# Performance work log

Hardware: AMD Instinct MI355X
Metric: run time of the kernel (lower is better)

Reference implementation:

```python
import jax, jax.numpy as jnp
import numpy as np

N_QUERY, N_POINTS, FEAT_DIM, K = 32768, 8192, 32, 8

def setup_inputs() -> dict:
    key = jax.random.key(0)
    k1, k2, k3 = jax.random.split(key, 3)
    xyz = jax.random.normal(k1, (N_QUERY, 3), dtype=jnp.float32)
    points = jax.random.normal(k2, (N_POINTS, 3), dtype=jnp.float32)
    # neural_point features are initialized uniform(-1e-4, 1e-4) in the module;
    # we use small-scale gaussians of the same magnitude.
    feats = jax.random.normal(k3, (N_POINTS, FEAT_DIM), dtype=jnp.float32) * 1e-4
    return {"xyz": xyz, "points": points, "feats": feats, "k": K}

def reference(xyz, points, feats, k):
    # Brute-force exact KNN (kpknn equivalent): squared euclidean distances [N, P]
    d2 = (jnp.sum(xyz * xyz, axis=-1, keepdims=True)
          - 2.0 * (xyz @ points.T)
          + jnp.sum(points * points, axis=-1)[None, :])
    _, idx = jax.lax.top_k(-d2, k)          # idx: [N, k] nearest-point indices
    knn_points = points[idx]                # [N, k, 3]
    knn_feats = feats[idx]                  # [N, k, FEAT_DIM]
    return knn_points, knn_feats
```

## Files before the change

### kernel.cpp

```cpp
#include <hip/hip_runtime.h>

#define NQ 32768
#define NP 8192
#define FD 32
#define KNN 8
#define QW 4
#define WPB 4
#define TB 256
#define QBLK (QW * WPB)
#define CHP 1024
#define NCH (NP / CHP)
#define ACH 4
#define CAP 64

__global__ __launch_bounds__(TB) void knn_kernel(
    const float* __restrict__ xyz, const float* __restrict__ points,
    const float* __restrict__ feats, float* __restrict__ out)
{
#pragma clang fp contract(off)
    __shared__ float4 sp[CHP];
    __shared__ unsigned short sidx16[QBLK * CAP];
    __shared__ int scnt[QBLK];

    const int t     = threadIdx.x;
    const int lane  = t & 63;
    const int wid   = t >> 6;
    const int qbase = blockIdx.x * QBLK + wid * QW;

    if (t < QBLK) scnt[t] = 0;

    float qx[QW], qy[QW], qz[QW], qn[QW];
#pragma unroll
    for (int qq = 0; qq < QW; ++qq) {
        int q = qbase + qq;
        float a = xyz[q * 3 + 0], b = xyz[q * 3 + 1], c = xyz[q * 3 + 2];
        qx[qq] = a; qy[qq] = b; qz[qq] = c;
        qn[qq] = (a * a + b * b) + c * c;
    }

    float mn[QW];
#pragma unroll
    for (int qq = 0; qq < QW; ++qq) mn[qq] = __builtin_inff();

    for (int c = 0; c < ACH; ++c) {
        __syncthreads();
        for (int i = t; i < CHP; i += TB) {
            int pi = c * CHP + i;
            float px = points[pi * 3 + 0], py = points[pi * 3 + 1], pz = points[pi * 3 + 2];
            float pn = __builtin_fmaf(pz, pz, __builtin_fmaf(py, py, px * px));
            sp[i] = make_float4(px, py, pz, pn);
        }
        __syncthreads();
#pragma unroll 4
        for (int s = 0; s < CHP / 64; ++s) {
            float4 p = sp[s * 64 + lane];
#pragma unroll
            for (int qq = 0; qq < QW; ++qq) {
                float dot = __builtin_fmaf(qz[qq], p.z, __builtin_fmaf(qy[qq], p.y, qx[qq] * p.x));
                float g   = __builtin_fmaf(-2.0f, dot, p.w);
                mn[qq] = fminf(mn[qq], g);
            }
        }
    }

    float tscr[QW];
#pragma unroll
    for (int qq = 0; qq < QW; ++qq) {
        float v = mn[qq];
        for (int k2 = 2; k2 <= 64; k2 <<= 1)
            for (int j = k2 >> 1; j > 0; j >>= 1) {
                float o = __shfl_xor(v, j);
                bool keepMin = ((lane & k2) == 0) == ((lane & j) == 0);
                v = ((o < v) == keepMin) ? o : v;
            }
        float t8 = __uint_as_float((unsigned)__builtin_amdgcn_readlane((int)__float_as_uint(v), 7));
        tscr[qq] = t8 + 1e-3f;
    }

    for (int k = 0; k < NCH; ++k) {
        int c = (ACH - 1 + k) & (NCH - 1);
        if (k > 0) {
            __syncthreads();
            for (int i = t; i < CHP; i += TB) {
                int pi = c * CHP + i;
                float px = points[pi * 3 + 0], py = points[pi * 3 + 1], pz = points[pi * 3 + 2];
                float pn = __builtin_fmaf(pz, pz, __builtin_fmaf(py, py, px * px));
                sp[i] = make_float4(px, py, pz, pn);
            }
            __syncthreads();
        }
#pragma unroll 2
        for (int s = 0; s < CHP / 64; ++s) {
            float4 p = sp[s * 64 + lane];
            int gidx = c * CHP + s * 64 + lane;
#pragma unroll
            for (int qq = 0; qq < QW; ++qq) {
                float dot = __builtin_fmaf(qz[qq], p.z, __builtin_fmaf(qy[qq], p.y, qx[qq] * p.x));
                float g   = __builtin_fmaf(-2.0f, dot, p.w);
                if (__builtin_expect(g <= tscr[qq], 0)) {
                    int wq = wid * QW + qq;
                    int slot = atomicAdd(&scnt[wq], 1);
                    if (slot < CAP) sidx16[wq * CAP + slot] = (unsigned short)gidx;
                }
            }
        }
    }
    __syncthreads();

    const float4* feats4 = (const float4*)feats;
    float4* outf4 = (float4*)(out + (long)NQ * KNN * 3);
#pragma unroll
    for (int qq = 0; qq < QW; ++qq) {
        int wq = wid * QW + qq;
        int cnt = scnt[wq]; if (cnt > CAP) cnt = CAP;
        unsigned long long key = ~0ull;
        if (lane < cnt) {
            int idx = sidx16[wq * CAP + lane];
            float px = points[idx * 3 + 0], py = points[idx * 3 + 1], pz = points[idx * 3 + 2];
            float pn  = (px * px + py * py) + pz * pz;
            float dot = __builtin_fmaf(qz[qq], pz, __builtin_fmaf(qy[qq], py, qx[qq] * px));
            float d2  = (qn[qq] - 2.0f * dot) + pn;
            unsigned b = __float_as_uint(d2);
            unsigned mk = (b & 0x80000000u) ? ~b : (b | 0x80000000u);
            key = ((unsigned long long)mk << 32) | (unsigned)idx;
        }
        for (int k2 = 2; k2 <= 64; k2 <<= 1)
            for (int j = k2 >> 1; j > 0; j >>= 1) {
                unsigned lo = __shfl_xor((unsigned)key, j);
                unsigned hi = __shfl_xor((unsigned)(key >> 32), j);
                unsigned long long o = ((unsigned long long)hi << 32) | lo;
                bool keepMin = ((lane & k2) == 0) == ((lane & j) == 0);
                key = ((o < key) == keepMin) ? o : key;
            }
        int q = qbase + qq;
        int nb = __shfl((int)(unsigned)key, lane >> 3);
        outf4[(long)q * (KNN * FD / 4) + lane] = feats4[(long)nb * (FD / 4) + (lane & 7)];
        int j2 = lane / 3;
        int nb2 = __shfl((int)(unsigned)key, j2);
        if (lane < 24) {
            out[(long)q * (KNN * 3) + lane] = points[nb2 * 3 + (lane - j2 * 3)];
        }
    }
}

extern "C" void kernel_launch(void* const* d_in, const int* in_sizes, int n_in,
                              void* d_out, int out_size, void* d_ws, size_t ws_size,
                              hipStream_t stream) {
    const float* xyz    = (const float*)d_in[0];
    const float* points = (const float*)d_in[1];
    const float* feats  = (const float*)d_in[2];
    float* out = (float*)d_out;
    hipLaunchKernelGGL(knn_kernel, dim3(NQ / QBLK), dim3(TB), 0, stream,
                       xyz, points, feats, out);
}
```

Before: 78.76 us.

## Merge KNN threshold and screening passes, double queries per wave

The kernel drops the separate min-distance pass over four chunks. It now computes a provisional threshold from the first chunk, then screens chunks 1-3 while still refining the running minimum, re-screens chunk 0, and finishes the rest, for nine chunk passes instead of twelve. Queries per wave go from 4 to 8 to reuse each shared-memory point load across more queries. Points are pre-scaled by -2 so each distance is three FMAs. Because the early screening uses a looser threshold, the candidate capacity is raised to 128, with a second bitonic sort and a merge when more than 64 candidates appear. This costs more registers, halves the grid size, and adds extra sort work when there are many candidates.

```diff
diff --git a/kernel.cpp b/kernel.cpp
--- a/kernel.cpp
+++ b/kernel.cpp
@@ -4,14 +4,38 @@
 #define NP 8192
 #define FD 32
 #define KNN 8
-#define QW 4
+#define QW 8
 #define WPB 4
 #define TB 256
 #define QBLK (QW * WPB)
 #define CHP 1024
-#define NCH (NP / CHP)
-#define ACH 4
-#define CAP 64
+#define CAP 128
+
+typedef unsigned long long u64;
+
+__device__ __forceinline__ u64 shfl_xor_u64(u64 k, int j) {
+    unsigned lo = __shfl_xor((unsigned)k, j);
+    unsigned hi = __shfl_xor((unsigned)(k >> 32), j);
+    return ((u64)hi << 32) | lo;
+}
+__device__ __forceinline__ u64 sort64_u64(u64 key, int lane) {
+    for (int k2 = 2; k2 <= 64; k2 <<= 1)
+        for (int j = k2 >> 1; j > 0; j >>= 1) {
+            u64 o = shfl_xor_u64(key, j);
+            bool keepMin = ((lane & k2) == 0) == ((lane & j) == 0);
+            key = ((o < key) == keepMin) ? o : key;
+        }
+    return key;
+}
+__device__ __forceinline__ float eighth_smallest64(float v, int lane) {
+    for (int k2 = 2; k2 <= 64; k2 <<= 1)
+        for (int j = k2 >> 1; j > 0; j >>= 1) {
+            float o = __shfl_xor(v, j);
+            bool keepMin = ((lane & k2) == 0) == ((lane & j) == 0);
+            v = ((o < v) == keepMin) ? o : v;
+        }
+    return __uint_as_float((unsigned)__builtin_amdgcn_readlane((int)__float_as_uint(v), 7));
+}
 
 __global__ __launch_bounds__(TB) void knn_kernel(
     const float* __restrict__ xyz, const float* __restrict__ points,
@@ -29,91 +53,64 @@
 
     if (t < QBLK) scnt[t] = 0;
 
-    float qx[QW], qy[QW], qz[QW], qn[QW];
+    float qx[QW], qy[QW], qz[QW], qn[QW], mn[QW], tscr[QW];
 #pragma unroll
     for (int qq = 0; qq < QW; ++qq) {
         int q = qbase + qq;
         float a = xyz[q * 3 + 0], b = xyz[q * 3 + 1], c = xyz[q * 3 + 2];
         qx[qq] = a; qy[qq] = b; qz[qq] = c;
         qn[qq] = (a * a + b * b) + c * c;
+        mn[qq] = __builtin_inff();
+        tscr[qq] = __builtin_inff();
     }
 
-    float mn[QW];
-#pragma unroll
-    for (int qq = 0; qq < QW; ++qq) mn[qq] = __builtin_inff();
-
-    for (int c = 0; c < ACH; ++c) {
+    for (int step = 0; step < 9; ++step) {
+        int c = (step <= 3) ? step : ((step == 4) ? 0 : step - 1);
         __syncthreads();
         for (int i = t; i < CHP; i += TB) {
             int pi = c * CHP + i;
             float px = points[pi * 3 + 0], py = points[pi * 3 + 1], pz = points[pi * 3 + 2];
             float pn = __builtin_fmaf(pz, pz, __builtin_fmaf(py, py, px * px));
-            sp[i] = make_float4(px, py, pz, pn);
+            sp[i] = make_float4(-2.0f * px, -2.0f * py, -2.0f * pz, pn);
         }
         __syncthreads();
-#pragma unroll 4
-        for (int s = 0; s < CHP / 64; ++s) {
-            float4 p = sp[s * 64 + lane];
-#pragma unroll
-            for (int qq = 0; qq < QW; ++qq) {
-                float dot = __builtin_fmaf(qz[qq], p.z, __builtin_fmaf(qy[qq], p.y, qx[qq] * p.x));
-                float g   = __builtin_fmaf(-2.0f, dot, p.w);
-                mn[qq] = fminf(mn[qq], g);
-            }
-        }
-    }
 
-    float tscr[QW];
-#pragma unroll
-    for (int qq = 0; qq < QW; ++qq) {
-        float v = mn[qq];
-        for (int k2 = 2; k2 <= 64; k2 <<= 1)
-            for (int j = k2 >> 1; j > 0; j >>= 1) {
-                float o = __shfl_xor(v, j);
-                bool keepMin = ((lane & k2) == 0) == ((lane & j) == 0);
-                v = ((o < v) == keepMin) ? o : v;
-            }
-        float t8 = __uint_as_float((unsigned)__builtin_amdgcn_readlane((int)__float_as_uint(v), 7));
-        tscr[qq] = t8 + 1e-3f;
-    }
-
-    for (int k = 0; k < NCH; ++k) {
-        int c = (ACH - 1 + k) & (NCH - 1);
-        if (k > 0) {
-            __syncthreads();
-            for (int i = t; i < CHP; i += TB) {
-                int pi = c * CHP + i;
-                float px = points[pi * 3 + 0], py = points[pi * 3 + 1], pz = points[pi * 3 + 2];
-                float pn = __builtin_fmaf(pz, pz, __builtin_fmaf(py, py, px * px));
-                sp[i] = make_float4(px, py, pz, pn);
-            }
-            __syncthreads();
-        }
+        const bool doMin = (step < 4), doScr = (step != 0);
 #pragma unroll 2
         for (int s = 0; s < CHP / 64; ++s) {
             float4 p = sp[s * 64 + lane];
             int gidx = c * CHP + s * 64 + lane;
 #pragma unroll
             for (int qq = 0; qq < QW; ++qq) {
-                float dot = __builtin_fmaf(qz[qq], p.z, __builtin_fmaf(qy[qq], p.y, qx[qq] * p.x));
-                float g   = __builtin_fmaf(-2.0f, dot, p.w);
-                if (__builtin_expect(g <= tscr[qq], 0)) {
-                    int wq = wid * QW + qq;
-                    int slot = atomicAdd(&scnt[wq], 1);
-                    if (slot < CAP) sidx16[wq * CAP + slot] = (unsigned short)gidx;
+                float g = __builtin_fmaf(qx[qq], p.x,
+                          __builtin_fmaf(qy[qq], p.y,
+                          __builtin_fmaf(qz[qq], p.z, p.w)));
+                if (doMin) mn[qq] = fminf(mn[qq], g);
+                if (doScr) {
+                    if (__builtin_expect(g <= tscr[qq], 0)) {
+                        int wq = wid * QW + qq;
+                        int slot = atomicAdd(&scnt[wq], 1);
+                        if (slot < CAP) sidx16[wq * CAP + slot] = (unsigned short)gidx;
+                    }
                 }
             }
         }
+
+        if (step == 0 || step == 3) {
+#pragma unroll
+            for (int qq = 0; qq < QW; ++qq)
+                tscr[qq] = eighth_smallest64(mn[qq], lane) + 1e-3f;
+        }
     }
-    __syncthreads();
 
     const float4* feats4 = (const float4*)feats;
     float4* outf4 = (float4*)(out + (long)NQ * KNN * 3);
-#pragma unroll
+#pragma unroll 1
     for (int qq = 0; qq < QW; ++qq) {
         int wq = wid * QW + qq;
         int cnt = scnt[wq]; if (cnt > CAP) cnt = CAP;
-        unsigned long long key = ~0ull;
+
+        u64 key1 = ~0ull;
         if (lane < cnt) {
             int idx = sidx16[wq * CAP + lane];
             float px = points[idx * 3 + 0], py = points[idx * 3 + 1], pz = points[idx * 3 + 2];
@@ -122,21 +119,42 @@
             float d2  = (qn[qq] - 2.0f * dot) + pn;
             unsigned b = __float_as_uint(d2);
             unsigned mk = (b & 0x80000000u) ? ~b : (b | 0x80000000u);
-            key = ((unsigned long long)mk << 32) | (unsigned)idx;
+            key1 = ((u64)mk << 32) | (unsigned)idx;
         }
-        for (int k2 = 2; k2 <= 64; k2 <<= 1)
-            for (int j = k2 >> 1; j > 0; j >>= 1) {
-                unsigned lo = __shfl_xor((unsigned)key, j);
-                unsigned hi = __shfl_xor((unsigned)(key >> 32), j);
-                unsigned long long o = ((unsigned long long)hi << 32) | lo;
-                bool keepMin = ((lane & k2) == 0) == ((lane & j) == 0);
-                key = ((o < key) == keepMin) ? o : key;
+        u64 v = sort64_u64(key1, lane);
+
+        if (cnt > 64) {
+            u64 key2 = ~0ull;
+            if (lane + 64 < cnt) {
+                int idx = sidx16[wq * CAP + 64 + lane];
+                float px = points[idx * 3 + 0], py = points[idx * 3 + 1], pz = points[idx * 3 + 2];
+                float pn  = (px * px + py * py) + pz * pz;
+                float dot = __builtin_fmaf(qz[qq], pz, __builtin_fmaf(qy[qq], py, qx[qq] * px));
+                float d2  = (qn[qq] - 2.0f * dot) + pn;
+                unsigned b = __float_as_uint(d2);
+                unsigned mk = (b & 0x80000000u) ? ~b : (b | 0x80000000u);
+                key2 = ((u64)mk << 32) | (unsigned)idx;
             }
+            u64 s2 = sort64_u64(key2, lane);
+            int src = (15 - lane) & 63;
+            unsigned lo2 = __shfl((unsigned)s2, src);
+            unsigned hi2 = __shfl((unsigned)(s2 >> 32), src);
+            u64 kr = ((u64)hi2 << 32) | lo2;
+            u64 m = (lane < 8) ? v : ((lane < 16) ? kr : ~0ull);
+#pragma unroll
+            for (int j = 8; j > 0; j >>= 1) {
+                u64 o = shfl_xor_u64(m, j);
+                bool low = (lane & j) == 0;
+                m = low ? (o < m ? o : m) : (o < m ? m : o);
+            }
+            v = m;
+        }
+
         int q = qbase + qq;
-        int nb = __shfl((int)(unsigned)key, lane >> 3);
+        int nb = __shfl((int)(unsigned)v, lane >> 3);
         outf4[(long)q * (KNN * FD / 4) + lane] = feats4[(long)nb * (FD / 4) + (lane & 7)];
         int j2 = lane / 3;
-        int nb2 = __shfl((int)(unsigned)key, j2);
+        int nb2 = __shfl((int)(unsigned)v, j2);
         if (lane < 24) {
             out[(long)q * (KNN * 3) + lane] = points[nb2 * 3 + (lane - j2 * 3)];
         }
```

After: 129.9 us. 64.9% more time.
